# Optimization experiments

Hardware: AMD Instinct MI355X
Metric: run time of the kernel (lower is better)

Reference implementation:

```python
import jax, jax.numpy as jnp
import numpy as np

B, N, D, P = 4, 4096, 64, 2
M, H = 64, 128
ARENA = 20.0  # positions uniform in [0, ARENA]^2; radius 1.0 -> ~32 neighbors


def _mlp2(x, Wa, ba, Wb, bb):
    return jax.nn.relu(x @ Wa + ba) @ Wb + bb


def setup_inputs() -> dict:
    key = jax.random.key(0)
    ks = jax.random.split(key, 14)
    def lin(k, fan_in, fan_out):
        bound = 1.0 / np.sqrt(fan_in)
        kw, kb = jax.random.split(k)
        W = jax.random.uniform(kw, (fan_in, fan_out), jnp.float32, -bound, bound)
        b = jax.random.uniform(kb, (fan_out,), jnp.float32, -bound, bound)
        return W, b
    W1, b1 = lin(ks[0], D, H)
    W2, b2 = lin(ks[1], H, M)
    W3, b3 = lin(ks[2], 2 * M, H)
    W4, b4 = lin(ks[3], H, M)
    W5, b5 = lin(ks[4], D + M, H)
    W6, b6 = lin(ks[5], H, D)
    agent_states = jax.random.normal(ks[6], (B, N, D), jnp.float32)
    agent_positions = jax.random.uniform(ks[7], (B, N, P), jnp.float32) * ARENA
    return {
        "agent_states": agent_states,
        "agent_positions": agent_positions,
        "neighbor_radius": 1,
        "W1": W1, "b1": b1, "W2": W2, "b2": b2,
        "W3": W3, "b3": b3, "W4": W4, "b4": b4,
        "W5": W5, "b5": b5, "W6": W6, "b6": b6,
    }


def reference(agent_states, agent_positions, neighbor_radius,
              W1, b1, W2, b2, W3, b3, W4, b4, W5, b5, W6, b6):
    n = agent_states.shape[1]
    # message encoder MLP: [B,N,D] -> [B,N,M]
    messages = _mlp2(agent_states, W1, b1, W2, b2)
    # dense pairwise distances [B,N,N] (faithful to original O(N^2) mask)
    diff = agent_positions[:, :, None, :] - agent_positions[:, None, :, :]
    distances = jnp.sqrt(jnp.sum(diff * diff, axis=-1))
    adj = (distances < jnp.float32(neighbor_radius)).astype(messages.dtype)
    adj = adj * (1.0 - jnp.eye(n, dtype=messages.dtype))[None]
    deg = jnp.clip(jnp.sum(adj, axis=-1, keepdims=True), 1.0, None)
    adj = adj / deg
    # vectorized form of the per-agent gather-aggregate loop
    aggregated = jnp.einsum('bij,bjm->bim', adj, messages)
    combined = jnp.concatenate([messages, aggregated], axis=-1)
    final_msgs = _mlp2(combined, W3, b3, W4, b4)
    feats = jnp.concatenate([agent_states, final_msgs], axis=-1)
    out = _mlp2(feats, W5, b5, W6, b6)
    return agent_states + out
```

## Files before the change

### kernel.cpp

```cpp
#include <hip/hip_runtime.h>

typedef unsigned short u16;
typedef __bf16 bf16x8 __attribute__((ext_vector_type(8)));
typedef unsigned short ushort8 __attribute__((ext_vector_type(8)));
typedef float f32x4 __attribute__((ext_vector_type(4)));

#define DEV_INLINE __device__ __forceinline__

constexpr int NB = 4;
constexpr int NAG = 4096;
constexpr int ROWS = NB * NAG;
constexpr int GRID = 20;
constexpr int CELLS = GRID * GRID;
constexpr int CSTRIDE = 404;
constexpr int MAXNB = 320;

DEV_INLINE u16 f2bu(float x) { __bf16 h = (__bf16)x; return __builtin_bit_cast(u16, h); }
DEV_INLINE float bu2f(u16 u) { return __builtin_bit_cast(float, ((unsigned)u) << 16); }

DEV_INLINE f32x4 MF(bf16x8 a, const u16* p, f32x4 c) {
  ushort8 bu = *(const ushort8*)p;
  return __builtin_amdgcn_mfma_f32_16x16x32_bf16(a, __builtin_bit_cast(bf16x8, bu), c, 0, 0, 0);
}

template<bool BF>
DEV_INLINE bf16x8 loadA(const void* __restrict__ src, int row, int c) {
  if constexpr (BF) {
    ushort8 u = *reinterpret_cast<const ushort8*>((const u16*)src + (size_t)row * 64 + c);
    return __builtin_bit_cast(bf16x8, u);
  } else {
    const float* f = (const float*)src + (size_t)row * 64 + c;
    f32x4 a = *(const f32x4*)f;
    f32x4 b = *(const f32x4*)(f + 4);
    bf16x8 r;
    r[0] = (__bf16)a[0]; r[1] = (__bf16)a[1]; r[2] = (__bf16)a[2]; r[3] = (__bf16)a[3];
    r[4] = (__bf16)b[0]; r[5] = (__bf16)b[1]; r[6] = (__bf16)b[2]; r[7] = (__bf16)b[3];
    return r;
  }
}

__global__ __launch_bounds__(256) void fused_setup_mlp1(
    const float* __restrict__ pos, const float* __restrict__ states,
    const float* __restrict__ W1, const float* __restrict__ b1,
    const float* __restrict__ W2, const float* __restrict__ b2,
    const float* __restrict__ W3, const float* __restrict__ W4,
    const float* __restrict__ W5, const float* __restrict__ W6,
    u16* __restrict__ wts, u16* __restrict__ msgs,
    float2* __restrict__ pos_sorted, int* __restrict__ cell_start,
    int* __restrict__ sid)
{
  extern __shared__ u16 smem[];
  const int tid = threadIdx.x;
  const int lane = tid & 63;
  const int wave = tid >> 6;

  if (blockIdx.x < NB) {
    int* cnt_s = (int*)smem;
    int* start_s = cnt_s + CELLS;
    u16* cell_of = (u16*)(start_s + CELLS + 1);
    u16* rank_of = cell_of + NAG;
    const int b = blockIdx.x;
    const float2* pb = (const float2*)(pos + (size_t)b * NAG * 2);
    for (int c = tid; c < CELLS; c += 256) cnt_s[c] = 0;
    __syncthreads();
    for (int i = tid; i < NAG; i += 256) {
      float2 p = pb[i];
      int cx = min(max((int)floorf(p.x), 0), GRID - 1);
      int cy = min(max((int)floorf(p.y), 0), GRID - 1);
      int c = cy * GRID + cx;
      rank_of[i] = (u16)atomicAdd(&cnt_s[c], 1);
      cell_of[i] = (u16)c;
    }
    __syncthreads();
    if (wave == 0) {
      int carry = 0;
      for (int g = 0; g < CELLS; g += 64) {
        int c = g + lane;
        int x = (c < CELLS) ? cnt_s[c] : 0;
#pragma unroll
        for (int off = 1; off < 64; off <<= 1) {
          int y = __shfl_up(x, off, 64);
          if (lane >= off) x += y;
        }
        if (c < CELLS) start_s[c + 1] = carry + x;
        carry += __shfl(x, 63, 64);
      }
      if (lane == 0) start_s[0] = 0;
    }
    __syncthreads();
    for (int c = tid; c <= CELLS; c += 256) cell_start[b * CSTRIDE + c] = start_s[c];
    for (int i = tid; i < NAG; i += 256) {
      int kk = start_s[cell_of[i]] + (int)rank_of[i];
      sid[b * NAG + kk] = b * NAG + i;
      pos_sorted[b * NAG + kk] = pb[i];
    }
    return;
  }

  if (blockIdx.x >= NB + 256) {
    const int base = (blockIdx.x - (NB + 256)) * 3072;
#pragma unroll
    for (int t = 0; t < 12; ++t) {
      int idx = base + t * 256 + tid;
      const float* src; int n, k, Nc;
      if (idx < 16384)      { src = W3; n = idx >> 7; k = idx & 127; Nc = 128; }
      else if (idx < 24576) { int li = idx - 16384; src = W4; n = li >> 7; k = li & 127; Nc = 64; }
      else if (idx < 40960) { int li = idx - 24576; src = W5; n = li >> 7; k = li & 127; Nc = 128; }
      else                  { int li = idx - 40960; src = W6; n = li >> 7; k = li & 127; Nc = 64; }
      wts[idx] = f2bu(src[k * Nc + n]);
    }
    return;
  }

  u16* WaTs = smem;
  u16* WbTs = smem + 128 * 72;
  u16* hs = WbTs + 64 * 136 + wave * (16 * 136);

  const int l15 = lane & 15;
  const int khalf = (lane >> 4) * 8;
  const int rb = (blockIdx.x - NB) * 64 + wave * 16;
  const int row = rb + l15;

  bf16x8 aS[2];
  aS[0] = loadA<false>(states, row, khalf);
  aS[1] = loadA<false>(states, row, 32 + khalf);

  for (int e = tid; e < 64 * 128; e += 256) {
    int n = e & 127, k = e >> 7;
    WaTs[n * 72 + k] = f2bu(W1[e]);
  }
  for (int e = tid; e < 128 * 64; e += 256) {
    int n = e & 63, k = e >> 6;
    WbTs[n * 136 + k] = f2bu(W2[e]);
  }
  __syncthreads();

  f32x4 acc1[8] = {};
#pragma unroll
  for (int kt = 0; kt < 2; ++kt) {
#pragma unroll
    for (int nt = 0; nt < 8; ++nt)
      acc1[nt] = MF(aS[kt], &WaTs[(nt * 16 + l15) * 72 + kt * 32 + khalf], acc1[nt]);
  }
#pragma unroll
  for (int nt = 0; nt < 8; ++nt) {
    const float bav = b1[nt * 16 + l15];
#pragma unroll
    for (int r = 0; r < 4; ++r)
      hs[((lane >> 4) * 4 + r) * 136 + nt * 16 + l15] = f2bu(fmaxf(acc1[nt][r] + bav, 0.0f));
  }
  f32x4 acc2[4] = {};
#pragma unroll
  for (int kt = 0; kt < 4; ++kt) {
    ushort8 au = *(const ushort8*)&hs[l15 * 136 + kt * 32 + khalf];
    bf16x8 a2 = __builtin_bit_cast(bf16x8, au);
#pragma unroll
    for (int nt = 0; nt < 4; ++nt)
      acc2[nt] = MF(a2, &WbTs[(nt * 16 + l15) * 136 + kt * 32 + khalf], acc2[nt]);
  }
#pragma unroll
  for (int nt = 0; nt < 4; ++nt) {
    const int gc = nt * 16 + l15;
    const float bbv = b2[gc];
#pragma unroll
    for (int r = 0; r < 4; ++r) {
      const int m = (lane >> 4) * 4 + r;
      msgs[(size_t)(rb + m) * 64 + gc] = f2bu(acc2[nt][r] + bbv);
    }
  }
}

__global__ __launch_bounds__(256) void agg_kernel(
    const float2* __restrict__ pos_sorted, const u16* __restrict__ msgs,
    const int* __restrict__ cell_start, const int* __restrict__ sid,
    const int* __restrict__ radius_ptr, u16* __restrict__ aggr)
{
  __shared__ u16 idxb[4][MAXNB];
  const int b = blockIdx.y;
  const int lane = threadIdx.x & 63;
  const int wave = threadIdx.x >> 6;
  const int k = blockIdx.x * 4 + wave;
  const float2* pb = pos_sorted + (size_t)b * NAG;
  const float2 pk = pb[k];
  const float r = (float)(*radius_ptr);
  const float r2 = __fmul_rn(r, r);
  const int cx = min(max((int)floorf(pk.x), 0), GRID - 1);
  const int cy = min(max((int)floorf(pk.y), 0), GRID - 1);
  const int* cs = cell_start + b * CSTRIDE;
  const int* sb = sid + b * NAG;
  const unsigned long long lt = (1ull << lane) - 1ull;

  int cnt = 0;
#pragma unroll
  for (int dy = -1; dy <= 1; ++dy) {
    const int yy = cy + dy;
    if (yy < 0 || yy >= GRID) continue;
    const int x0 = max(cx - 1, 0), x1 = min(cx + 1, GRID - 1);
    const int c0 = cs[yy * GRID + x0];
    const int c1 = cs[yy * GRID + x1 + 1];
    for (int base = c0; base < c1; base += 64) {
      const int j = base + lane;
      bool ok = false;
      if (j < c1) {
        const float2 pj = pb[j];
        const float dx_ = pk.x - pj.x;
        const float dy_ = pk.y - pj.y;
        const float d2 = __fadd_rn(__fmul_rn(dx_, dx_), __fmul_rn(dy_, dy_));
        ok = (d2 < r2) && (j != k);
      }
      const unsigned long long m = __ballot(ok);
      if (ok) {
        const int p = cnt + __popcll(m & lt);
        if (p < MAXNB) idxb[wave][p] = (u16)sb[j];
      }
      cnt += (int)__popcll(m);
    }
  }

  float acc = 0.0f;
  const int n = min(cnt, MAXNB);
  for (int g = 0; g < n; g += 8) {
    ushort8 ii = *(const ushort8*)&idxb[wave][g];
    float vs[8];
#pragma unroll
    for (int s = 0; s < 8; ++s) {
      const int jj = (g + s < n) ? (int)ii[s] : (int)ii[0];
      vs[s] = bu2f(msgs[(size_t)jj * 64 + lane]);
    }
#pragma unroll
    for (int s = 0; s < 8; ++s) acc += (g + s < n) ? vs[s] : 0.0f;
  }
  const float inv = 1.0f / (float)(cnt > 0 ? cnt : 1);
  const int orow = sb[k];
  aggr[(size_t)orow * 64 + lane] = f2bu(acc * inv);
}

__global__ __launch_bounds__(1024, 4) void mlp23_kernel(
    const float* __restrict__ states, const u16* __restrict__ msgs,
    const u16* __restrict__ aggr, const u16* __restrict__ wts,
    const float* __restrict__ b3, const float* __restrict__ b4,
    const float* __restrict__ b5, const float* __restrict__ b6,
    float* __restrict__ out)
{
  extern __shared__ u16 smem[];
  u16* W3s = smem;
  u16* W4s = W3s + 128 * 136;
  u16* W5s = W4s + 64 * 136;
  u16* W6s = W5s + 128 * 136;
  u16* hsb = W6s + 64 * 136;
  u16* fsb = hsb + 4 * 16 * 136;

  const int tid = threadIdx.x;
  const int lane = tid & 63;
  const int wave = tid >> 6;
  const int rg = wave >> 2;
  const int cq = wave & 3;
  const int l15 = lane & 15;
  const int khalf = (lane >> 4) * 8;
  const int rb = blockIdx.x * 64 + rg * 16;
  const int row = rb + l15;
  u16* hs = hsb + rg * (16 * 136);
  u16* fs = fsb + rg * (16 * 136);

  bf16x8 aM[2], aG[2], aS[2];
  aM[0] = loadA<true>(msgs, row, khalf);
  aM[1] = loadA<true>(msgs, row, 32 + khalf);
  aG[0] = loadA<true>(aggr, row, khalf);
  aG[1] = loadA<true>(aggr, row, 32 + khalf);
  aS[0] = loadA<false>(states, row, khalf);
  aS[1] = loadA<false>(states, row, 32 + khalf);

  for (int t = tid; t < 6144; t += 1024) {
    const int e = t * 8;
    ushort8 v = *(const ushort8*)&wts[e];
    u16* dst;
    if (e < 16384)      dst = &W3s[(e >> 7) * 136 + (e & 127)];
    else if (e < 24576) { int li = e - 16384; dst = &W4s[(li >> 7) * 136 + (li & 127)]; }
    else if (e < 40960) { int li = e - 24576; dst = &W5s[(li >> 7) * 136 + (li & 127)]; }
    else                { int li = e - 40960; dst = &W6s[(li >> 7) * 136 + (li & 127)]; }
    *(ushort8*)dst = v;
  }
  __syncthreads();

  f32x4 acc1[2] = {};
#pragma unroll
  for (int kt = 0; kt < 4; ++kt) {
    bf16x8 a = (kt < 2) ? aM[kt] : aG[kt - 2];
#pragma unroll
    for (int j = 0; j < 2; ++j) {
      const int nt = cq * 2 + j;
      acc1[j] = MF(a, &W3s[(nt * 16 + l15) * 136 + kt * 32 + khalf], acc1[j]);
    }
  }
#pragma unroll
  for (int j = 0; j < 2; ++j) {
    const int col = (cq * 2 + j) * 16 + l15;
    const float bv = b3[col];
#pragma unroll
    for (int r = 0; r < 4; ++r)
      hs[((lane >> 4) * 4 + r) * 136 + col] = f2bu(fmaxf(acc1[j][r] + bv, 0.0f));
  }
  __syncthreads();

  f32x4 acc2 = {};
#pragma unroll
  for (int kt = 0; kt < 4; ++kt) {
    ushort8 au = *(const ushort8*)&hs[l15 * 136 + kt * 32 + khalf];
    acc2 = MF(__builtin_bit_cast(bf16x8, au),
              &W4s[(cq * 16 + l15) * 136 + kt * 32 + khalf], acc2);
  }
  {
    const int col = cq * 16 + l15;
    const float bv = b4[col];
#pragma unroll
    for (int r = 0; r < 4; ++r)
      fs[((lane >> 4) * 4 + r) * 136 + col] = f2bu(acc2[r] + bv);
  }
  __syncthreads();

  f32x4 acc3[2] = {};
#pragma unroll
  for (int kt = 0; kt < 4; ++kt) {
    bf16x8 a;
    if (kt < 2) a = aS[kt];
    else {
      ushort8 au = *(const ushort8*)&fs[l15 * 136 + (kt - 2) * 32 + khalf];
      a = __builtin_bit_cast(bf16x8, au);
    }
#pragma unroll
    for (int j = 0; j < 2; ++j) {
      const int nt = cq * 2 + j;
      acc3[j] = MF(a, &W5s[(nt * 16 + l15) * 136 + kt * 32 + khalf], acc3[j]);
    }
  }
#pragma unroll
  for (int j = 0; j < 2; ++j) {
    const int col = (cq * 2 + j) * 16 + l15;
    const float bv = b5[col];
#pragma unroll
    for (int r = 0; r < 4; ++r)
      hs[((lane >> 4) * 4 + r) * 136 + col] = f2bu(fmaxf(acc3[j][r] + bv, 0.0f));
  }
  __syncthreads();

  f32x4 acc4 = {};
#pragma unroll
  for (int kt = 0; kt < 4; ++kt) {
    ushort8 au = *(const ushort8*)&hs[l15 * 136 + kt * 32 + khalf];
    acc4 = MF(__builtin_bit_cast(bf16x8, au),
              &W6s[(cq * 16 + l15) * 136 + kt * 32 + khalf], acc4);
  }
  {
    const int col = cq * 16 + l15;
    const float bv = b6[col];
#pragma unroll
    for (int r = 0; r < 4; ++r) {
      const int m = (lane >> 4) * 4 + r;
      const size_t o = (size_t)(rb + m) * 64 + col;
      out[o] = acc4[r] + bv + states[o];
    }
  }
}

extern "C" void kernel_launch(void* const* d_in, const int* in_sizes, int n_in,
                              void* d_out, int out_size, void* d_ws, size_t ws_size,
                              hipStream_t stream) {
  const float* states = (const float*)d_in[0];
  const float* pos    = (const float*)d_in[1];
  const int*   radius = (const int*)d_in[2];
  const float* W1 = (const float*)d_in[3];
  const float* b1 = (const float*)d_in[4];
  const float* W2 = (const float*)d_in[5];
  const float* b2 = (const float*)d_in[6];
  const float* W3 = (const float*)d_in[7];
  const float* b3 = (const float*)d_in[8];
  const float* W4 = (const float*)d_in[9];
  const float* b4 = (const float*)d_in[10];
  const float* W5 = (const float*)d_in[11];
  const float* b5 = (const float*)d_in[12];
  const float* W6 = (const float*)d_in[13];
  const float* b6 = (const float*)d_in[14];
  float* out = (float*)d_out;

  u16* ws16 = (u16*)d_ws;
  u16* msgs = ws16;
  u16* aggr = msgs + (size_t)ROWS * 64;
  u16* wts  = aggr + (size_t)ROWS * 64;
  char* pbyte = (char*)(wts + 49152);
  float2* pos_sorted = (float2*)pbyte;
  int* cell_start = (int*)(pbyte + (size_t)ROWS * 8);
  int* sid = cell_start + NB * CSTRIDE;

  constexpr int LDS_K1 = (128 * 72 + 64 * 136 + 4 * 16 * 136) * 2;
  constexpr int LDS_K3 = (384 * 136 + 8 * 16 * 136) * 2;

  fused_setup_mlp1<<<NB + 256 + 16, 256, LDS_K1, stream>>>(
      pos, states, W1, b1, W2, b2, W3, W4, W5, W6,
      wts, msgs, pos_sorted, cell_start, sid);

  agg_kernel<<<dim3(NAG / 4, NB), 256, 0, stream>>>(
      pos_sorted, msgs, cell_start, sid, radius, aggr);

  mlp23_kernel<<<ROWS / 64, 1024, LDS_K3, stream>>>(
      states, msgs, aggr, wts, b3, b4, b5, b6, out);
}
```

Measured before the change: 42.34 us.

## Fuse three kernels into one cooperative persistent kernel with grid syncs

Merges the setup/MLP1, neighbor aggregation and MLP2/3 kernels into a single cooperative launch of 256 blocks of 1024 threads. Grid-wide barriers separate the phases, and W3-W6 are staged into LDS once before the aggregation phase. W1/W2 are now pre-transposed to bf16 in global memory. Each wave aggregates four agents and the neighbor buffer shrinks to 256 entries. This removes kernel launch gaps and repeated weight staging, at the cost of grid.sync overhead, lower occupancy (one 1024-thread block with about 154KB LDS per CU) and a lower neighbor cap.

New measurement: 139.1 us. 3.28x slower.

```diff
diff --git a/kernel.cpp b/kernel.cpp
--- a/kernel.cpp
+++ b/kernel.cpp
@@ -1,4 +1,7 @@
 #include <hip/hip_runtime.h>
+#include <hip/hip_cooperative_groups.h>
+
+namespace cg = cooperative_groups;
 
 typedef unsigned short u16;
 typedef __bf16 bf16x8 __attribute__((ext_vector_type(8)));
@@ -13,7 +16,7 @@
 constexpr int GRID = 20;
 constexpr int CELLS = GRID * GRID;
 constexpr int CSTRIDE = 404;
-constexpr int MAXNB = 320;
+constexpr int MAXNB = 256;
 
 DEV_INLINE u16 f2bu(float x) { __bf16 h = (__bf16)x; return __builtin_bit_cast(u16, h); }
 DEV_INLINE float bu2f(u16 u) { return __builtin_bit_cast(float, ((unsigned)u) << 16); }
@@ -39,31 +42,36 @@
   }
 }
 
-__global__ __launch_bounds__(256) void fused_setup_mlp1(
-    const float* __restrict__ pos, const float* __restrict__ states,
+
+__global__ __launch_bounds__(1024) void mono_kernel(
+    const float* __restrict__ states, const float* __restrict__ pos,
+    const int* __restrict__ radius_ptr,
     const float* __restrict__ W1, const float* __restrict__ b1,
     const float* __restrict__ W2, const float* __restrict__ b2,
-    const float* __restrict__ W3, const float* __restrict__ W4,
-    const float* __restrict__ W5, const float* __restrict__ W6,
-    u16* __restrict__ wts, u16* __restrict__ msgs,
+    const float* __restrict__ W3, const float* __restrict__ b3,
+    const float* __restrict__ W4, const float* __restrict__ b4,
+    const float* __restrict__ W5, const float* __restrict__ b5,
+    const float* __restrict__ W6, const float* __restrict__ b6,
+    u16* __restrict__ wts, u16* __restrict__ msgs, u16* __restrict__ aggr,
     float2* __restrict__ pos_sorted, int* __restrict__ cell_start,
-    int* __restrict__ sid)
+    int* __restrict__ sid, float* __restrict__ out)
 {
   extern __shared__ u16 smem[];
+  cg::grid_group grid = cg::this_grid();
   const int tid = threadIdx.x;
   const int lane = tid & 63;
   const int wave = tid >> 6;
-
-  if (blockIdx.x < NB) {
+  const int bid = blockIdx.x;
+
+  if (bid < NB) {
     int* cnt_s = (int*)smem;
     int* start_s = cnt_s + CELLS;
     u16* cell_of = (u16*)(start_s + CELLS + 1);
     u16* rank_of = cell_of + NAG;
-    const int b = blockIdx.x;
-    const float2* pb = (const float2*)(pos + (size_t)b * NAG * 2);
-    for (int c = tid; c < CELLS; c += 256) cnt_s[c] = 0;
-    __syncthreads();
-    for (int i = tid; i < NAG; i += 256) {
+    const float2* pb = (const float2*)(pos + (size_t)bid * NAG * 2);
+    for (int c = tid; c < CELLS; c += 1024) cnt_s[c] = 0;
+    __syncthreads();
+    for (int i = tid; i < NAG; i += 1024) {
       float2 p = pb[i];
       int cx = min(max((int)floorf(p.x), 0), GRID - 1);
       int cy = min(max((int)floorf(p.y), 0), GRID - 1);
@@ -88,189 +96,50 @@
       if (lane == 0) start_s[0] = 0;
     }
     __syncthreads();
-    for (int c = tid; c <= CELLS; c += 256) cell_start[b * CSTRIDE + c] = start_s[c];
-    for (int i = tid; i < NAG; i += 256) {
+    for (int c = tid; c <= CELLS; c += 1024) cell_start[bid * CSTRIDE + c] = start_s[c];
+    for (int i = tid; i < NAG; i += 1024) {
       int kk = start_s[cell_of[i]] + (int)rank_of[i];
-      sid[b * NAG + kk] = b * NAG + i;
-      pos_sorted[b * NAG + kk] = pb[i];
-    }
-    return;
-  }
-
-  if (blockIdx.x >= NB + 256) {
-    const int base = (blockIdx.x - (NB + 256)) * 3072;
-#pragma unroll
-    for (int t = 0; t < 12; ++t) {
-      int idx = base + t * 256 + tid;
-      const float* src; int n, k, Nc;
-      if (idx < 16384)      { src = W3; n = idx >> 7; k = idx & 127; Nc = 128; }
-      else if (idx < 24576) { int li = idx - 16384; src = W4; n = li >> 7; k = li & 127; Nc = 64; }
-      else if (idx < 40960) { int li = idx - 24576; src = W5; n = li >> 7; k = li & 127; Nc = 128; }
-      else                  { int li = idx - 40960; src = W6; n = li >> 7; k = li & 127; Nc = 64; }
-      wts[idx] = f2bu(src[k * Nc + n]);
-    }
-    return;
-  }
-
-  u16* WaTs = smem;
-  u16* WbTs = smem + 128 * 72;
-  u16* hs = WbTs + 64 * 136 + wave * (16 * 136);
+      sid[bid * NAG + kk] = bid * NAG + i;
+      pos_sorted[bid * NAG + kk] = pb[i];
+    }
+  } else if (bid < NB + 64) {
+    const int idx = (bid - NB) * 1024 + tid;
+    const float* src; int li, Nc;
+    if (idx < 16384)      { src = W3; li = idx;          Nc = 128; }
+    else if (idx < 24576) { src = W4; li = idx - 16384;  Nc = 64;  }
+    else if (idx < 40960) { src = W5; li = idx - 24576;  Nc = 128; }
+    else if (idx < 49152) { src = W6; li = idx - 40960;  Nc = 64;  }
+    else if (idx < 57344) { src = W1; li = idx - 49152;  Nc = 128; }
+    else                  { src = W2; li = idx - 57344;  Nc = 64;  }
+    const bool w1 = (idx >= 49152) && (idx < 57344);
+    const int n = w1 ? (li >> 6) : (li >> 7);
+    const int k = w1 ? (li & 63) : (li & 127);
+    wts[idx] = f2bu(src[k * Nc + n]);
+  }
+  grid.sync();
+
+  u16* W3s = smem;
+  u16* W4s = smem + 17408;
+  u16* W5s = smem + 26112;
+  u16* W6s = smem + 43520;
+  u16* reg2 = smem + 52224;
 
   const int l15 = lane & 15;
   const int khalf = (lane >> 4) * 8;
-  const int rb = (blockIdx.x - NB) * 64 + wave * 16;
+  const int rg = wave >> 2;
+  const int cq = wave & 3;
+  const int rb = bid * 64 + rg * 16;
   const int row = rb + l15;
 
   bf16x8 aS[2];
   aS[0] = loadA<false>(states, row, khalf);
   aS[1] = loadA<false>(states, row, 32 + khalf);
 
-  for (int e = tid; e < 64 * 128; e += 256) {
-    int n = e & 127, k = e >> 7;
-    WaTs[n * 72 + k] = f2bu(W1[e]);
-  }
-  for (int e = tid; e < 128 * 64; e += 256) {
-    int n = e & 63, k = e >> 6;
-    WbTs[n * 136 + k] = f2bu(W2[e]);
-  }
-  __syncthreads();
-
-  f32x4 acc1[8] = {};
-#pragma unroll
-  for (int kt = 0; kt < 2; ++kt) {
-#pragma unroll
-    for (int nt = 0; nt < 8; ++nt)
-      acc1[nt] = MF(aS[kt], &WaTs[(nt * 16 + l15) * 72 + kt * 32 + khalf], acc1[nt]);
-  }
-#pragma unroll
-  for (int nt = 0; nt < 8; ++nt) {
-    const float bav = b1[nt * 16 + l15];
-#pragma unroll
-    for (int r = 0; r < 4; ++r)
-      hs[((lane >> 4) * 4 + r) * 136 + nt * 16 + l15] = f2bu(fmaxf(acc1[nt][r] + bav, 0.0f));
-  }
-  f32x4 acc2[4] = {};
-#pragma unroll
-  for (int kt = 0; kt < 4; ++kt) {
-    ushort8 au = *(const ushort8*)&hs[l15 * 136 + kt * 32 + khalf];
-    bf16x8 a2 = __builtin_bit_cast(bf16x8, au);
-#pragma unroll
-    for (int nt = 0; nt < 4; ++nt)
-      acc2[nt] = MF(a2, &WbTs[(nt * 16 + l15) * 136 + kt * 32 + khalf], acc2[nt]);
-  }
-#pragma unroll
-  for (int nt = 0; nt < 4; ++nt) {
-    const int gc = nt * 16 + l15;
-    const float bbv = b2[gc];
-#pragma unroll
-    for (int r = 0; r < 4; ++r) {
-      const int m = (lane >> 4) * 4 + r;
-      msgs[(size_t)(rb + m) * 64 + gc] = f2bu(acc2[nt][r] + bbv);
-    }
-  }
-}
-
-__global__ __launch_bounds__(256) void agg_kernel(
-    const float2* __restrict__ pos_sorted, const u16* __restrict__ msgs,
-    const int* __restrict__ cell_start, const int* __restrict__ sid,
-    const int* __restrict__ radius_ptr, u16* __restrict__ aggr)
-{
-  __shared__ u16 idxb[4][MAXNB];
-  const int b = blockIdx.y;
-  const int lane = threadIdx.x & 63;
-  const int wave = threadIdx.x >> 6;
-  const int k = blockIdx.x * 4 + wave;
-  const float2* pb = pos_sorted + (size_t)b * NAG;
-  const float2 pk = pb[k];
-  const float r = (float)(*radius_ptr);
-  const float r2 = __fmul_rn(r, r);
-  const int cx = min(max((int)floorf(pk.x), 0), GRID - 1);
-  const int cy = min(max((int)floorf(pk.y), 0), GRID - 1);
-  const int* cs = cell_start + b * CSTRIDE;
-  const int* sb = sid + b * NAG;
-  const unsigned long long lt = (1ull << lane) - 1ull;
-
-  int cnt = 0;
-#pragma unroll
-  for (int dy = -1; dy <= 1; ++dy) {
-    const int yy = cy + dy;
-    if (yy < 0 || yy >= GRID) continue;
-    const int x0 = max(cx - 1, 0), x1 = min(cx + 1, GRID - 1);
-    const int c0 = cs[yy * GRID + x0];
-    const int c1 = cs[yy * GRID + x1 + 1];
-    for (int base = c0; base < c1; base += 64) {
-      const int j = base + lane;
-      bool ok = false;
-      if (j < c1) {
-        const float2 pj = pb[j];
-        const float dx_ = pk.x - pj.x;
-        const float dy_ = pk.y - pj.y;
-        const float d2 = __fadd_rn(__fmul_rn(dx_, dx_), __fmul_rn(dy_, dy_));
-        ok = (d2 < r2) && (j != k);
-      }
-      const unsigned long long m = __ballot(ok);
-      if (ok) {
-        const int p = cnt + __popcll(m & lt);
-        if (p < MAXNB) idxb[wave][p] = (u16)sb[j];
-      }
-      cnt += (int)__popcll(m);
-    }
-  }
-
-  float acc = 0.0f;
-  const int n = min(cnt, MAXNB);
-  for (int g = 0; g < n; g += 8) {
-    ushort8 ii = *(const ushort8*)&idxb[wave][g];
-    float vs[8];
-#pragma unroll
-    for (int s = 0; s < 8; ++s) {
-      const int jj = (g + s < n) ? (int)ii[s] : (int)ii[0];
-      vs[s] = bu2f(msgs[(size_t)jj * 64 + lane]);
-    }
-#pragma unroll
-    for (int s = 0; s < 8; ++s) acc += (g + s < n) ? vs[s] : 0.0f;
-  }
-  const float inv = 1.0f / (float)(cnt > 0 ? cnt : 1);
-  const int orow = sb[k];
-  aggr[(size_t)orow * 64 + lane] = f2bu(acc * inv);
-}
-
-__global__ __launch_bounds__(1024, 4) void mlp23_kernel(
-    const float* __restrict__ states, const u16* __restrict__ msgs,
-    const u16* __restrict__ aggr, const u16* __restrict__ wts,
-    const float* __restrict__ b3, const float* __restrict__ b4,
-    const float* __restrict__ b5, const float* __restrict__ b6,
-    float* __restrict__ out)
-{
-  extern __shared__ u16 smem[];
-  u16* W3s = smem;
-  u16* W4s = W3s + 128 * 136;
-  u16* W5s = W4s + 64 * 136;
-  u16* W6s = W5s + 128 * 136;
-  u16* hsb = W6s + 64 * 136;
-  u16* fsb = hsb + 4 * 16 * 136;
-
-  const int tid = threadIdx.x;
-  const int lane = tid & 63;
-  const int wave = tid >> 6;
-  const int rg = wave >> 2;
-  const int cq = wave & 3;
-  const int l15 = lane & 15;
-  const int khalf = (lane >> 4) * 8;
-  const int rb = blockIdx.x * 64 + rg * 16;
-  const int row = rb + l15;
-  u16* hs = hsb + rg * (16 * 136);
-  u16* fs = fsb + rg * (16 * 136);
-
-  bf16x8 aM[2], aG[2], aS[2];
-  aM[0] = loadA<true>(msgs, row, khalf);
-  aM[1] = loadA<true>(msgs, row, 32 + khalf);
-  aG[0] = loadA<true>(aggr, row, khalf);
-  aG[1] = loadA<true>(aggr, row, 32 + khalf);
-  aS[0] = loadA<false>(states, row, khalf);
-  aS[1] = loadA<false>(states, row, 32 + khalf);
-
-  for (int t = tid; t < 6144; t += 1024) {
+  u16* W1Ts = reg2;
+  u16* W2Ts = reg2 + 9216;
+  u16* hs1  = reg2 + 17920 + rg * 2176;
+
+  for (int t = tid; t < 6528; t += 1024) {
     const int e = t * 8;
     ushort8 v = *(const ushort8*)&wts[e];
     u16* dst;
@@ -280,84 +149,199 @@
     else                { int li = e - 40960; dst = &W6s[(li >> 7) * 136 + (li & 127)]; }
     *(ushort8*)dst = v;
   }
+  {
+    const int e = tid * 8;
+    ushort8 v1 = *(const ushort8*)&wts[49152 + e];
+    *(ushort8*)&W1Ts[(e >> 6) * 72 + (e & 63)] = v1;
+    ushort8 v2 = *(const ushort8*)&wts[57344 + e];
+    *(ushort8*)&W2Ts[(e >> 7) * 136 + (e & 127)] = v2;
+  }
   __syncthreads();
 
-  f32x4 acc1[2] = {};
-#pragma unroll
-  for (int kt = 0; kt < 4; ++kt) {
-    bf16x8 a = (kt < 2) ? aM[kt] : aG[kt - 2];
+  {
+    f32x4 acc1[2] = {};
+#pragma unroll
+    for (int kt = 0; kt < 2; ++kt) {
+#pragma unroll
+      for (int j = 0; j < 2; ++j) {
+        const int nt = cq * 2 + j;
+        acc1[j] = MF(aS[kt], &W1Ts[(nt * 16 + l15) * 72 + kt * 32 + khalf], acc1[j]);
+      }
+    }
 #pragma unroll
     for (int j = 0; j < 2; ++j) {
-      const int nt = cq * 2 + j;
-      acc1[j] = MF(a, &W3s[(nt * 16 + l15) * 136 + kt * 32 + khalf], acc1[j]);
-    }
-  }
-#pragma unroll
-  for (int j = 0; j < 2; ++j) {
-    const int col = (cq * 2 + j) * 16 + l15;
-    const float bv = b3[col];
+      const int col = (cq * 2 + j) * 16 + l15;
+      const float bv = b1[col];
+#pragma unroll
+      for (int r = 0; r < 4; ++r)
+        hs1[((lane >> 4) * 4 + r) * 136 + col] = f2bu(fmaxf(acc1[j][r] + bv, 0.0f));
+    }
+    __syncthreads();
+    f32x4 acc2 = {};
+#pragma unroll
+    for (int kt = 0; kt < 4; ++kt) {
+      ushort8 au = *(const ushort8*)&hs1[l15 * 136 + kt * 32 + khalf];
+      acc2 = MF(__builtin_bit_cast(bf16x8, au),
+                &W2Ts[(cq * 16 + l15) * 136 + kt * 32 + khalf], acc2);
+    }
+    const int col = cq * 16 + l15;
+    const float bv = b2[col];
 #pragma unroll
     for (int r = 0; r < 4; ++r)
-      hs[((lane >> 4) * 4 + r) * 136 + col] = f2bu(fmaxf(acc1[j][r] + bv, 0.0f));
-  }
-  __syncthreads();
-
-  f32x4 acc2 = {};
-#pragma unroll
-  for (int kt = 0; kt < 4; ++kt) {
-    ushort8 au = *(const ushort8*)&hs[l15 * 136 + kt * 32 + khalf];
-    acc2 = MF(__builtin_bit_cast(bf16x8, au),
-              &W4s[(cq * 16 + l15) * 136 + kt * 32 + khalf], acc2);
-  }
+      msgs[(size_t)(rb + (lane >> 4) * 4 + r) * 64 + col] = f2bu(acc2[r] + bv);
+  }
+  grid.sync();
+
   {
-    const int col = cq * 16 + l15;
-    const float bv = b4[col];
-#pragma unroll
-    for (int r = 0; r < 4; ++r)
-      fs[((lane >> 4) * 4 + r) * 136 + col] = f2bu(acc2[r] + bv);
-  }
-  __syncthreads();
-
-  f32x4 acc3[2] = {};
-#pragma unroll
-  for (int kt = 0; kt < 4; ++kt) {
-    bf16x8 a;
-    if (kt < 2) a = aS[kt];
-    else {
-      ushort8 au = *(const ushort8*)&fs[l15 * 136 + (kt - 2) * 32 + khalf];
-      a = __builtin_bit_cast(bf16x8, au);
+    const float r = (float)(*radius_ptr);
+    const float r2 = __fmul_rn(r, r);
+    const unsigned long long lt = (1ull << lane) - 1ull;
+    u16* idxw = reg2 + wave * (4 * MAXNB);
+    const int wv = bid * 16 + wave;
+#pragma unroll 1
+    for (int a = 0; a < 4; ++a) {
+      const int kg = wv * 4 + a;
+      const int b = kg >> 12;
+      const int kl = kg & (NAG - 1);
+      const float2* pb = pos_sorted + (size_t)b * NAG;
+      const float2 pk = pb[kl];
+      const int cx = min(max((int)floorf(pk.x), 0), GRID - 1);
+      const int cy = min(max((int)floorf(pk.y), 0), GRID - 1);
+      const int* cs = cell_start + b * CSTRIDE;
+      const int* sb = sid + b * NAG;
+      int cnt = 0;
+#pragma unroll
+      for (int dy = -1; dy <= 1; ++dy) {
+        const int yy = cy + dy;
+        if (yy < 0 || yy >= GRID) continue;
+        const int x0 = max(cx - 1, 0), x1 = min(cx + 1, GRID - 1);
+        const int c0 = cs[yy * GRID + x0];
+        const int c1 = cs[yy * GRID + x1 + 1];
+        for (int base = c0; base < c1; base += 64) {
+          const int j = base + lane;
+          bool ok = false;
+          if (j < c1) {
+            const float2 pj = pb[j];
+            const float dx_ = pk.x - pj.x;
+            const float dy_ = pk.y - pj.y;
+            const float d2 = __fadd_rn(__fmul_rn(dx_, dx_), __fmul_rn(dy_, dy_));
+            ok = (d2 < r2) && (j != kl);
+          }
+          const unsigned long long m = __ballot(ok);
+          if (ok) {
+            const int p = cnt + __popcll(m & lt);
+            if (p < MAXNB) idxw[a * MAXNB + p] = (u16)sb[j];
+          }
+          cnt += (int)__popcll(m);
+        }
+      }
+      float acc = 0.0f;
+      const int n = min(cnt, MAXNB);
+      for (int g = 0; g < n; g += 8) {
+        ushort8 ii = *(const ushort8*)&idxw[a * MAXNB + g];
+        float vs[8];
+#pragma unroll
+        for (int s = 0; s < 8; ++s) {
+          const int jj = (g + s < n) ? (int)ii[s] : (int)ii[0];
+          vs[s] = bu2f(msgs[(size_t)jj * 64 + lane]);
+        }
+#pragma unroll
+        for (int s = 0; s < 8; ++s) acc += (g + s < n) ? vs[s] : 0.0f;
+      }
+      const float inv = 1.0f / (float)(cnt > 0 ? cnt : 1);
+      aggr[(size_t)sb[kl] * 64 + lane] = f2bu(acc * inv);
+    }
+  }
+  grid.sync();
+
+  {
+    u16* hs = reg2 + rg * 2176;
+    u16* fs = reg2 + 8704 + rg * 2176;
+
+    bf16x8 aM[2], aG[2];
+    aM[0] = loadA<true>(msgs, row, khalf);
+    aM[1] = loadA<true>(msgs, row, 32 + khalf);
+    aG[0] = loadA<true>(aggr, row, khalf);
+    aG[1] = loadA<true>(aggr, row, 32 + khalf);
+
+    f32x4 acc1[2] = {};
+#pragma unroll
+    for (int kt = 0; kt < 4; ++kt) {
+      bf16x8 a = (kt < 2) ? aM[kt] : aG[kt - 2];
+#pragma unroll
+      for (int j = 0; j < 2; ++j) {
+        const int nt = cq * 2 + j;
+        acc1[j] = MF(a, &W3s[(nt * 16 + l15) * 136 + kt * 32 + khalf], acc1[j]);
+      }
     }
 #pragma unroll
     for (int j = 0; j < 2; ++j) {
-      const int nt = cq * 2 + j;
-      acc3[j] = MF(a, &W5s[(nt * 16 + l15) * 136 + kt * 32 + khalf], acc3[j]);
-    }
-  }
-#pragma unroll
-  for (int j = 0; j < 2; ++j) {
-    const int col = (cq * 2 + j) * 16 + l15;
-    const float bv = b5[col];
-#pragma unroll
-    for (int r = 0; r < 4; ++r)
-      hs[((lane >> 4) * 4 + r) * 136 + col] = f2bu(fmaxf(acc3[j][r] + bv, 0.0f));
-  }
-  __syncthreads();
-
-  f32x4 acc4 = {};
-#pragma unroll
-  for (int kt = 0; kt < 4; ++kt) {
-    ushort8 au = *(const ushort8*)&hs[l15 * 136 + kt * 32 + khalf];
-    acc4 = MF(__builtin_bit_cast(bf16x8, au),
-              &W6s[(cq * 16 + l15) * 136 + kt * 32 + khalf], acc4);
-  }
-  {
-    const int col = cq * 16 + l15;
-    const float bv = b6[col];
-#pragma unroll
-    for (int r = 0; r < 4; ++r) {
-      const int m = (lane >> 4) * 4 + r;
-      const size_t o = (size_t)(rb + m) * 64 + col;
-      out[o] = acc4[r] + bv + states[o];
+      const int col = (cq * 2 + j) * 16 + l15;
+      const float bv = b3[col];
+#pragma unroll
+      for (int r = 0; r < 4; ++r)
+        hs[((lane >> 4) * 4 + r) * 136 + col] = f2bu(fmaxf(acc1[j][r] + bv, 0.0f));
+    }
+    __syncthreads();
+
+    f32x4 acc2 = {};
+#pragma unroll
+    for (int kt = 0; kt < 4; ++kt) {
+      ushort8 au = *(const ushort8*)&hs[l15 * 136 + kt * 32 + khalf];
+      acc2 = MF(__builtin_bit_cast(bf16x8, au),
+                &W4s[(cq * 16 + l15) * 136 + kt * 32 + khalf], acc2);
+    }
+    {
+      const int col = cq * 16 + l15;
+      const float bv = b4[col];
+#pragma unroll
+      for (int r = 0; r < 4; ++r)
+        fs[((lane >> 4) * 4 + r) * 136 + col] = f2bu(acc2[r] + bv);
+    }
+    __syncthreads();
+
+    f32x4 acc3[2] = {};
+#pragma unroll
+    for (int kt = 0; kt < 4; ++kt) {
+      bf16x8 a;
+      if (kt < 2) a = aS[kt];
+      else {
+        ushort8 au = *(const ushort8*)&fs[l15 * 136 + (kt - 2) * 32 + khalf];
+        a = __builtin_bit_cast(bf16x8, au);
+      }
+#pragma unroll
+      for (int j = 0; j < 2; ++j) {
+        const int nt = cq * 2 + j;
+        acc3[j] = MF(a, &W5s[(nt * 16 + l15) * 136 + kt * 32 + khalf], acc3[j]);
+      }
+    }
+    __syncthreads();
+#pragma unroll
+    for (int j = 0; j < 2; ++j) {
+      const int col = (cq * 2 + j) * 16 + l15;
+      const float bv = b5[col];
+#pragma unroll
+      for (int r = 0; r < 4; ++r)
+        hs[((lane >> 4) * 4 + r) * 136 + col] = f2bu(fmaxf(acc3[j][r] + bv, 0.0f));
+    }
+    __syncthreads();
+
+    f32x4 acc4 = {};
+#pragma unroll
+    for (int kt = 0; kt < 4; ++kt) {
+      ushort8 au = *(const ushort8*)&hs[l15 * 136 + kt * 32 + khalf];
+      acc4 = MF(__builtin_bit_cast(bf16x8, au),
+                &W6s[(cq * 16 + l15) * 136 + kt * 32 + khalf], acc4);
+    }
+    {
+      const int col = cq * 16 + l15;
+      const float bv = b6[col];
+#pragma unroll
+      for (int r = 0; r < 4; ++r) {
+        const int m = (lane >> 4) * 4 + r;
+        const size_t o = (size_t)(rb + m) * 64 + col;
+        out[o] = acc4[r] + bv + states[o];
+      }
     }
   }
 }
@@ -386,21 +370,21 @@
   u16* msgs = ws16;
   u16* aggr = msgs + (size_t)ROWS * 64;
   u16* wts  = aggr + (size_t)ROWS * 64;
-  char* pbyte = (char*)(wts + 49152);
+  char* pbyte = (char*)(wts + 65536);
   float2* pos_sorted = (float2*)pbyte;
   int* cell_start = (int*)(pbyte + (size_t)ROWS * 8);
   int* sid = cell_start + NB * CSTRIDE;
 
-  constexpr int LDS_K1 = (128 * 72 + 64 * 136 + 4 * 16 * 136) * 2;
-  constexpr int LDS_K3 = (384 * 136 + 8 * 16 * 136) * 2;
-
-  fused_setup_mlp1<<<NB + 256 + 16, 256, LDS_K1, stream>>>(
-      pos, states, W1, b1, W2, b2, W3, W4, W5, W6,
-      wts, msgs, pos_sorted, cell_start, sid);
-
-  agg_kernel<<<dim3(NAG / 4, NB), 256, 0, stream>>>(
-      pos_sorted, msgs, cell_start, sid, radius, aggr);
-
-  mlp23_kernel<<<ROWS / 64, 1024, LDS_K3, stream>>>(
-      states, msgs, aggr, wts, b3, b4, b5, b6, out);
+  constexpr unsigned LDS_BYTES = 78848u * 2u;
+
+  void* args[] = {
+    (void*)&states, (void*)&pos, (void*)&radius,
+    (void*)&W1, (void*)&b1, (void*)&W2, (void*)&b2,
+    (void*)&W3, (void*)&b3, (void*)&W4, (void*)&b4,
+    (void*)&W5, (void*)&b5, (void*)&W6, (void*)&b6,
+    (void*)&wts, (void*)&msgs, (void*)&aggr,
+    (void*)&pos_sorted, (void*)&cell_start, (void*)&sid, (void*)&out
+  };
+  hipLaunchCooperativeKernel((void*)mono_kernel, dim3(256), dim3(1024),
+                             args, LDS_BYTES, stream);
 }
```

## Fuse neighbor aggregation into the post-MLP kernel and vectorize weight staging

Applied to the files above, without the earlier changes.

Removes the standalone aggregation kernel. Each wave of the MLP kernel now computes neighbor aggregates for four of the block's rows, writing them to shared memory instead of a global aggr buffer. This saves a launch and a global round trip, and lets the aggregation gather overlap with weight staging. The per-agent neighbor cap drops to 256 to fit LDS, an extra barrier protects the reused scratch buffers, and W1/W2 transposed staging now uses float4 loads. The risks are higher LDS use (~148KB) with 1024-thread blocks, less parallelism in aggregation (256 large blocks), and possible truncation above 256 neighbors.

Result: slower. 44.19 us (+4.4%).

```diff
diff --git a/kernel.cpp b/kernel.cpp
--- a/kernel.cpp
+++ b/kernel.cpp
@@ -13,7 +13,7 @@
 constexpr int GRID = 20;
 constexpr int CELLS = GRID * GRID;
 constexpr int CSTRIDE = 404;
-constexpr int MAXNB = 320;
+constexpr int MAXNB = 256;
 
 DEV_INLINE u16 f2bu(float x) { __bf16 h = (__bf16)x; return __builtin_bit_cast(u16, h); }
 DEV_INLINE float bu2f(u16 u) { return __builtin_bit_cast(float, ((unsigned)u) << 16); }
@@ -125,13 +125,19 @@
   aS[0] = loadA<false>(states, row, khalf);
   aS[1] = loadA<false>(states, row, 32 + khalf);
 
-  for (int e = tid; e < 64 * 128; e += 256) {
-    int n = e & 127, k = e >> 7;
-    WaTs[n * 72 + k] = f2bu(W1[e]);
-  }
-  for (int e = tid; e < 128 * 64; e += 256) {
-    int n = e & 63, k = e >> 6;
-    WbTs[n * 136 + k] = f2bu(W2[e]);
+  for (int t = tid; t < 2048; t += 256) {
+    const int e = t * 4;
+    f32x4 v = *(const f32x4*)&W1[e];
+    const int k = e >> 7, n = e & 127;
+#pragma unroll
+    for (int i = 0; i < 4; ++i) WaTs[(n + i) * 72 + k] = f2bu(v[i]);
+  }
+  for (int t = tid; t < 2048; t += 256) {
+    const int e = t * 4;
+    f32x4 v = *(const f32x4*)&W2[e];
+    const int k = e >> 6, n = e & 63;
+#pragma unroll
+    for (int i = 0; i < 4; ++i) WbTs[(n + i) * 136 + k] = f2bu(v[i]);
   }
   __syncthreads();
 
@@ -170,85 +176,22 @@
   }
 }
 
-__global__ __launch_bounds__(256) void agg_kernel(
-    const float2* __restrict__ pos_sorted, const u16* __restrict__ msgs,
-    const int* __restrict__ cell_start, const int* __restrict__ sid,
-    const int* __restrict__ radius_ptr, u16* __restrict__ aggr)
-{
-  __shared__ u16 idxb[4][MAXNB];
-  const int b = blockIdx.y;
-  const int lane = threadIdx.x & 63;
-  const int wave = threadIdx.x >> 6;
-  const int k = blockIdx.x * 4 + wave;
-  const float2* pb = pos_sorted + (size_t)b * NAG;
-  const float2 pk = pb[k];
-  const float r = (float)(*radius_ptr);
-  const float r2 = __fmul_rn(r, r);
-  const int cx = min(max((int)floorf(pk.x), 0), GRID - 1);
-  const int cy = min(max((int)floorf(pk.y), 0), GRID - 1);
-  const int* cs = cell_start + b * CSTRIDE;
-  const int* sb = sid + b * NAG;
-  const unsigned long long lt = (1ull << lane) - 1ull;
-
-  int cnt = 0;
-#pragma unroll
-  for (int dy = -1; dy <= 1; ++dy) {
-    const int yy = cy + dy;
-    if (yy < 0 || yy >= GRID) continue;
-    const int x0 = max(cx - 1, 0), x1 = min(cx + 1, GRID - 1);
-    const int c0 = cs[yy * GRID + x0];
-    const int c1 = cs[yy * GRID + x1 + 1];
-    for (int base = c0; base < c1; base += 64) {
-      const int j = base + lane;
-      bool ok = false;
-      if (j < c1) {
-        const float2 pj = pb[j];
-        const float dx_ = pk.x - pj.x;
-        const float dy_ = pk.y - pj.y;
-        const float d2 = __fadd_rn(__fmul_rn(dx_, dx_), __fmul_rn(dy_, dy_));
-        ok = (d2 < r2) && (j != k);
-      }
-      const unsigned long long m = __ballot(ok);
-      if (ok) {
-        const int p = cnt + __popcll(m & lt);
-        if (p < MAXNB) idxb[wave][p] = (u16)sb[j];
-      }
-      cnt += (int)__popcll(m);
-    }
-  }
-
-  float acc = 0.0f;
-  const int n = min(cnt, MAXNB);
-  for (int g = 0; g < n; g += 8) {
-    ushort8 ii = *(const ushort8*)&idxb[wave][g];
-    float vs[8];
-#pragma unroll
-    for (int s = 0; s < 8; ++s) {
-      const int jj = (g + s < n) ? (int)ii[s] : (int)ii[0];
-      vs[s] = bu2f(msgs[(size_t)jj * 64 + lane]);
-    }
-#pragma unroll
-    for (int s = 0; s < 8; ++s) acc += (g + s < n) ? vs[s] : 0.0f;
-  }
-  const float inv = 1.0f / (float)(cnt > 0 ? cnt : 1);
-  const int orow = sb[k];
-  aggr[(size_t)orow * 64 + lane] = f2bu(acc * inv);
-}
-
-__global__ __launch_bounds__(1024, 4) void mlp23_kernel(
-    const float* __restrict__ states, const u16* __restrict__ msgs,
-    const u16* __restrict__ aggr, const u16* __restrict__ wts,
+__global__ __launch_bounds__(1024, 4) void agg_mlp23_kernel(
+    const float* __restrict__ states, const float* __restrict__ pos,
+    const u16* __restrict__ msgs, const u16* __restrict__ wts,
+    const float2* __restrict__ pos_sorted, const int* __restrict__ cell_start,
+    const int* __restrict__ sid, const int* __restrict__ radius_ptr,
     const float* __restrict__ b3, const float* __restrict__ b4,
     const float* __restrict__ b5, const float* __restrict__ b6,
     float* __restrict__ out)
 {
   extern __shared__ u16 smem[];
   u16* W3s = smem;
-  u16* W4s = W3s + 128 * 136;
-  u16* W5s = W4s + 64 * 136;
-  u16* W6s = W5s + 128 * 136;
-  u16* hsb = W6s + 64 * 136;
-  u16* fsb = hsb + 4 * 16 * 136;
+  u16* W4s = smem + 17408;
+  u16* W5s = smem + 26112;
+  u16* W6s = smem + 43520;
+  u16* agg_s = smem + 52224;
+  u16* dynr = smem + 56832;
 
   const int tid = threadIdx.x;
   const int lane = tid & 63;
@@ -257,16 +200,13 @@
   const int cq = wave & 3;
   const int l15 = lane & 15;
   const int khalf = (lane >> 4) * 8;
-  const int rb = blockIdx.x * 64 + rg * 16;
+  const int rb0 = blockIdx.x * 64;
+  const int rb = rb0 + rg * 16;
   const int row = rb + l15;
-  u16* hs = hsb + rg * (16 * 136);
-  u16* fs = fsb + rg * (16 * 136);
-
-  bf16x8 aM[2], aG[2], aS[2];
+
+  bf16x8 aM[2], aS[2];
   aM[0] = loadA<true>(msgs, row, khalf);
   aM[1] = loadA<true>(msgs, row, 32 + khalf);
-  aG[0] = loadA<true>(aggr, row, khalf);
-  aG[1] = loadA<true>(aggr, row, 32 + khalf);
   aS[0] = loadA<false>(states, row, khalf);
   aS[1] = loadA<false>(states, row, 32 + khalf);
 
@@ -280,12 +220,81 @@
     else                { int li = e - 40960; dst = &W6s[(li >> 7) * 136 + (li & 127)]; }
     *(ushort8*)dst = v;
   }
-  __syncthreads();
+
+  {
+    const float r = (float)(*radius_ptr);
+    const float r2 = __fmul_rn(r, r);
+    const unsigned long long lt = (1ull << lane) - 1ull;
+    u16* idxw = dynr + wave * 1024;
+#pragma unroll 1
+    for (int a = 0; a < 4; ++a) {
+      const int gi = rb0 + wave * 4 + a;
+      const int b = gi >> 12;
+      const int il = gi & (NAG - 1);
+      const float2 pk = ((const float2*)pos)[(size_t)b * NAG + il];
+      const int cx = min(max((int)floorf(pk.x), 0), GRID - 1);
+      const int cy = min(max((int)floorf(pk.y), 0), GRID - 1);
+      const int* cs = cell_start + b * CSTRIDE;
+      const int* sb = sid + b * NAG;
+      const float2* pb = pos_sorted + (size_t)b * NAG;
+      int cnt = 0;
+#pragma unroll
+      for (int dy = -1; dy <= 1; ++dy) {
+        const int yy = cy + dy;
+        if (yy < 0 || yy >= GRID) continue;
+        const int x0 = max(cx - 1, 0), x1 = min(cx + 1, GRID - 1);
+        const int c0 = cs[yy * GRID + x0];
+        const int c1 = cs[yy * GRID + x1 + 1];
+        for (int base = c0; base < c1; base += 64) {
+          const int j = base + lane;
+          bool ok = false; int sbj = 0;
+          if (j < c1) {
+            const float2 pj = pb[j];
+            sbj = sb[j];
+            const float dx_ = pk.x - pj.x;
+            const float dy_ = pk.y - pj.y;
+            const float d2 = __fadd_rn(__fmul_rn(dx_, dx_), __fmul_rn(dy_, dy_));
+            ok = (d2 < r2) && (sbj != gi);
+          }
+          const unsigned long long m = __ballot(ok);
+          if (ok) {
+            const int p = cnt + __popcll(m & lt);
+            if (p < MAXNB) idxw[a * MAXNB + p] = (u16)sbj;
+          }
+          cnt += (int)__popcll(m);
+        }
+      }
+      float acc = 0.0f;
+      const int n = min(cnt, MAXNB);
+      for (int g = 0; g < n; g += 8) {
+        ushort8 ii = *(const ushort8*)&idxw[a * MAXNB + g];
+        float vs[8];
+#pragma unroll
+        for (int s = 0; s < 8; ++s) {
+          const int jj = (g + s < n) ? (int)ii[s] : (int)ii[0];
+          vs[s] = bu2f(msgs[(size_t)jj * 64 + lane]);
+        }
+#pragma unroll
+        for (int s = 0; s < 8; ++s) acc += (g + s < n) ? vs[s] : 0.0f;
+      }
+      const float inv = 1.0f / (float)(cnt > 0 ? cnt : 1);
+      agg_s[(wave * 4 + a) * 72 + lane] = f2bu(acc * inv);
+    }
+  }
+  __syncthreads();
+
+  u16* hs = dynr + rg * 2176;
+  u16* fs = dynr + 8704 + rg * 2176;
 
   f32x4 acc1[2] = {};
 #pragma unroll
   for (int kt = 0; kt < 4; ++kt) {
-    bf16x8 a = (kt < 2) ? aM[kt] : aG[kt - 2];
+    bf16x8 a;
+    if (kt < 2) a = aM[kt];
+    else {
+      ushort8 au = *(const ushort8*)&agg_s[(rg * 16 + l15) * 72 + (kt - 2) * 32 + khalf];
+      a = __builtin_bit_cast(bf16x8, au);
+    }
 #pragma unroll
     for (int j = 0; j < 2; ++j) {
       const int nt = cq * 2 + j;
@@ -333,6 +342,7 @@
       acc3[j] = MF(a, &W5s[(nt * 16 + l15) * 136 + kt * 32 + khalf], acc3[j]);
     }
   }
+  __syncthreads();
 #pragma unroll
   for (int j = 0; j < 2; ++j) {
     const int col = (cq * 2 + j) * 16 + l15;
@@ -384,23 +394,20 @@
 
   u16* ws16 = (u16*)d_ws;
   u16* msgs = ws16;
-  u16* aggr = msgs + (size_t)ROWS * 64;
-  u16* wts  = aggr + (size_t)ROWS * 64;
+  u16* wts  = msgs + (size_t)ROWS * 64;
   char* pbyte = (char*)(wts + 49152);
   float2* pos_sorted = (float2*)pbyte;
   int* cell_start = (int*)(pbyte + (size_t)ROWS * 8);
   int* sid = cell_start + NB * CSTRIDE;
 
   constexpr int LDS_K1 = (128 * 72 + 64 * 136 + 4 * 16 * 136) * 2;
-  constexpr int LDS_K3 = (384 * 136 + 8 * 16 * 136) * 2;
+  constexpr int LDS_K2 = 74240 * 2;
 
   fused_setup_mlp1<<<NB + 256 + 16, 256, LDS_K1, stream>>>(
       pos, states, W1, b1, W2, b2, W3, W4, W5, W6,
       wts, msgs, pos_sorted, cell_start, sid);
 
-  agg_kernel<<<dim3(NAG / 4, NB), 256, 0, stream>>>(
-      pos_sorted, msgs, cell_start, sid, radius, aggr);
-
-  mlp23_kernel<<<ROWS / 64, 1024, LDS_K3, stream>>>(
-      states, msgs, aggr, wts, b3, b4, b5, b6, out);
+  agg_mlp23_kernel<<<256, 1024, LDS_K2, stream>>>(
+      states, pos, msgs, wts, pos_sorted, cell_start, sid, radius,
+      b3, b4, b5, b6, out);
 }
```

## Use 1024-thread blocks in setup/MLP1 kernel with coalesced weight transpose via LDS

Applied to the files above, without the earlier changes.

Grows the fused setup/MLP1 kernel to 1024 threads per block. The message MLP now splits output columns across 4 waves per 16-row group instead of one wave doing all columns, and the per-block W1/W2 bf16 transpose loads float2 coalesced into an LDS staging buffer before transposing. The binning and weight-conversion blocks scale their strides accordingly, so fewer conversion blocks are launched. This cuts per-thread weight-staging work and serial MFMA chains, at the cost of extra barriers and a larger block footprint. MAXNB is also lowered from 320 to 256, which shrinks the aggregation kernel's index buffer but risks overflow for dense neighbourhoods.

New measurement: 42.64 us. About the same (+0.7%).

```diff
diff --git a/kernel.cpp b/kernel.cpp
--- a/kernel.cpp
+++ b/kernel.cpp
@@ -1,6 +1,7 @@
 #include <hip/hip_runtime.h>
 
 typedef unsigned short u16;
+typedef unsigned int u32;
 typedef __bf16 bf16x8 __attribute__((ext_vector_type(8)));
 typedef unsigned short ushort8 __attribute__((ext_vector_type(8)));
 typedef float f32x4 __attribute__((ext_vector_type(4)));
@@ -13,10 +14,11 @@
 constexpr int GRID = 20;
 constexpr int CELLS = GRID * GRID;
 constexpr int CSTRIDE = 404;
-constexpr int MAXNB = 320;
+constexpr int MAXNB = 256;
 
 DEV_INLINE u16 f2bu(float x) { __bf16 h = (__bf16)x; return __builtin_bit_cast(u16, h); }
-DEV_INLINE float bu2f(u16 u) { return __builtin_bit_cast(float, ((unsigned)u) << 16); }
+DEV_INLINE float bu2f(u16 u) { return __builtin_bit_cast(float, ((u32)u) << 16); }
+DEV_INLINE u32 pack2(float a, float b) { return (u32)f2bu(a) | ((u32)f2bu(b) << 16); }
 
 DEV_INLINE f32x4 MF(bf16x8 a, const u16* p, f32x4 c) {
   ushort8 bu = *(const ushort8*)p;
@@ -39,7 +41,7 @@
   }
 }
 
-__global__ __launch_bounds__(256) void fused_setup_mlp1(
+__global__ __launch_bounds__(1024) void fused_setup_mlp1(
     const float* __restrict__ pos, const float* __restrict__ states,
     const float* __restrict__ W1, const float* __restrict__ b1,
     const float* __restrict__ W2, const float* __restrict__ b2,
@@ -53,17 +55,17 @@
   const int tid = threadIdx.x;
   const int lane = tid & 63;
   const int wave = tid >> 6;
-
-  if (blockIdx.x < NB) {
+  const int bid = blockIdx.x;
+
+  if (bid < NB) {
     int* cnt_s = (int*)smem;
     int* start_s = cnt_s + CELLS;
     u16* cell_of = (u16*)(start_s + CELLS + 1);
     u16* rank_of = cell_of + NAG;
-    const int b = blockIdx.x;
-    const float2* pb = (const float2*)(pos + (size_t)b * NAG * 2);
-    for (int c = tid; c < CELLS; c += 256) cnt_s[c] = 0;
+    const float2* pb = (const float2*)(pos + (size_t)bid * NAG * 2);
+    for (int c = tid; c < CELLS; c += 1024) cnt_s[c] = 0;
     __syncthreads();
-    for (int i = tid; i < NAG; i += 256) {
+    for (int i = tid; i < NAG; i += 1024) {
       float2 p = pb[i];
       int cx = min(max((int)floorf(p.x), 0), GRID - 1);
       int cy = min(max((int)floorf(p.y), 0), GRID - 1);
@@ -88,20 +90,20 @@
       if (lane == 0) start_s[0] = 0;
     }
     __syncthreads();
-    for (int c = tid; c <= CELLS; c += 256) cell_start[b * CSTRIDE + c] = start_s[c];
-    for (int i = tid; i < NAG; i += 256) {
+    for (int c = tid; c <= CELLS; c += 1024) cell_start[bid * CSTRIDE + c] = start_s[c];
+    for (int i = tid; i < NAG; i += 1024) {
       int kk = start_s[cell_of[i]] + (int)rank_of[i];
-      sid[b * NAG + kk] = b * NAG + i;
-      pos_sorted[b * NAG + kk] = pb[i];
+      sid[bid * NAG + kk] = bid * NAG + i;
+      pos_sorted[bid * NAG + kk] = pb[i];
     }
     return;
   }
 
-  if (blockIdx.x >= NB + 256) {
-    const int base = (blockIdx.x - (NB + 256)) * 3072;
+  if (bid >= NB + 256) {
+    const int base = (bid - (NB + 256)) * 12288;
 #pragma unroll
     for (int t = 0; t < 12; ++t) {
-      int idx = base + t * 256 + tid;
+      int idx = base + t * 1024 + tid;
       const float* src; int n, k, Nc;
       if (idx < 16384)      { src = W3; n = idx >> 7; k = idx & 127; Nc = 128; }
       else if (idx < 24576) { int li = idx - 16384; src = W4; n = li >> 7; k = li & 127; Nc = 64; }
@@ -113,60 +115,85 @@
   }
 
   u16* WaTs = smem;
-  u16* WbTs = smem + 128 * 72;
-  u16* hs = WbTs + 64 * 136 + wave * (16 * 136);
+  u16* WbTs = smem + 9216;
+  u16* ovl  = smem + 17920;
 
   const int l15 = lane & 15;
   const int khalf = (lane >> 4) * 8;
-  const int rb = (blockIdx.x - NB) * 64 + wave * 16;
+  const int rg = wave >> 2;
+  const int cq = wave & 3;
+  const int rb = (bid - NB) * 64 + rg * 16;
   const int row = rb + l15;
 
   bf16x8 aS[2];
   aS[0] = loadA<false>(states, row, khalf);
   aS[1] = loadA<false>(states, row, 32 + khalf);
 
-  for (int e = tid; e < 64 * 128; e += 256) {
-    int n = e & 127, k = e >> 7;
-    WaTs[n * 72 + k] = f2bu(W1[e]);
-  }
-  for (int e = tid; e < 128 * 64; e += 256) {
-    int n = e & 63, k = e >> 6;
-    WbTs[n * 136 + k] = f2bu(W2[e]);
-  }
-  __syncthreads();
-
-  f32x4 acc1[8] = {};
+  for (int t = tid; t < 4096; t += 1024) {
+    const int e = t * 2;
+    const int k = e >> 7, n = e & 127;
+    const float2 v = *(const float2*)&W1[e];
+    *(u32*)&ovl[k * 132 + n] = pack2(v.x, v.y);
+  }
+  __syncthreads();
+  {
+    const int n = tid & 127, g = tid >> 7;
+    ushort8 v;
+#pragma unroll
+    for (int j = 0; j < 8; ++j) v[j] = ovl[(g * 8 + j) * 132 + n];
+    *(ushort8*)&WaTs[n * 72 + g * 8] = v;
+  }
+  __syncthreads();
+  for (int t = tid; t < 4096; t += 1024) {
+    const int e = t * 2;
+    const int k = e >> 6, n = e & 63;
+    const float2 v = *(const float2*)&W2[e];
+    *(u32*)&ovl[k * 68 + n] = pack2(v.x, v.y);
+  }
+  __syncthreads();
+  {
+    const int n = tid & 63, g = tid >> 6;
+    ushort8 v;
+#pragma unroll
+    for (int j = 0; j < 8; ++j) v[j] = ovl[(g * 8 + j) * 68 + n];
+    *(ushort8*)&WbTs[n * 136 + g * 8] = v;
+  }
+  __syncthreads();
+
+  u16* hs = ovl + rg * 2176;
+
+  f32x4 acc1[2] = {};
 #pragma unroll
   for (int kt = 0; kt < 2; ++kt) {
 #pragma unroll
-    for (int nt = 0; nt < 8; ++nt)
-      acc1[nt] = MF(aS[kt], &WaTs[(nt * 16 + l15) * 72 + kt * 32 + khalf], acc1[nt]);
-  }
-#pragma unroll
-  for (int nt = 0; nt < 8; ++nt) {
-    const float bav = b1[nt * 16 + l15];
+    for (int j = 0; j < 2; ++j) {
+      const int nt = cq * 2 + j;
+      acc1[j] = MF(aS[kt], &WaTs[(nt * 16 + l15) * 72 + kt * 32 + khalf], acc1[j]);
+    }
+  }
+#pragma unroll
+  for (int j = 0; j < 2; ++j) {
+    const int col = (cq * 2 + j) * 16 + l15;
+    const float bv = b1[col];
 #pragma unroll
     for (int r = 0; r < 4; ++r)
-      hs[((lane >> 4) * 4 + r) * 136 + nt * 16 + l15] = f2bu(fmaxf(acc1[nt][r] + bav, 0.0f));
-  }
-  f32x4 acc2[4] = {};
+      hs[((lane >> 4) * 4 + r) * 136 + col] = f2bu(fmaxf(acc1[j][r] + bv, 0.0f));
+  }
+  __syncthreads();
+
+  f32x4 acc2 = {};
 #pragma unroll
   for (int kt = 0; kt < 4; ++kt) {
     ushort8 au = *(const ushort8*)&hs[l15 * 136 + kt * 32 + khalf];
-    bf16x8 a2 = __builtin_bit_cast(bf16x8, au);
-#pragma unroll
-    for (int nt = 0; nt < 4; ++nt)
-      acc2[nt] = MF(a2, &WbTs[(nt * 16 + l15) * 136 + kt * 32 + khalf], acc2[nt]);
-  }
-#pragma unroll
-  for (int nt = 0; nt < 4; ++nt) {
-    const int gc = nt * 16 + l15;
-    const float bbv = b2[gc];
-#pragma unroll
-    for (int r = 0; r < 4; ++r) {
-      const int m = (lane >> 4) * 4 + r;
-      msgs[(size_t)(rb + m) * 64 + gc] = f2bu(acc2[nt][r] + bbv);
-    }
+    acc2 = MF(__builtin_bit_cast(bf16x8, au),
+              &WbTs[(cq * 16 + l15) * 136 + kt * 32 + khalf], acc2);
+  }
+  {
+    const int col = cq * 16 + l15;
+    const float bv = b2[col];
+#pragma unroll
+    for (int r = 0; r < 4; ++r)
+      msgs[(size_t)(rb + (lane >> 4) * 4 + r) * 64 + col] = f2bu(acc2[r] + bv);
   }
 }
 
@@ -391,10 +418,10 @@
   int* cell_start = (int*)(pbyte + (size_t)ROWS * 8);
   int* sid = cell_start + NB * CSTRIDE;
 
-  constexpr int LDS_K1 = (128 * 72 + 64 * 136 + 4 * 16 * 136) * 2;
+  constexpr int LDS_K1 = 26624 * 2;
   constexpr int LDS_K3 = (384 * 136 + 8 * 16 * 136) * 2;
 
-  fused_setup_mlp1<<<NB + 256 + 16, 256, LDS_K1, stream>>>(
+  fused_setup_mlp1<<<NB + 256 + 4, 1024, LDS_K1, stream>>>(
       pos, states, W1, b1, W2, b2, W3, W4, W5, W6,
       wts, msgs, pos_sorted, cell_start, sid);
 
```
